# Optimization experiments

Hardware: AMD Instinct MI355X
Metric: run time of the kernel (lower is better)

Reference implementation:

```python
import jax, jax.numpy as jnp
import numpy as np

B, S, D = 4, 2048, 1024
H, A = 16, 64  # num_heads, attention_depth
LN_EPS = 1e-3  # keras LayerNormalization default epsilon


def setup_inputs() -> dict:
    key = jax.random.key(0)
    ks = jax.random.split(key, 12)
    s_in = 1.0 / np.sqrt(D)
    return {
        "query_inputs": jax.random.normal(ks[0], (B, S, D), jnp.float32),
        "key_value_inputs": jax.random.normal(ks[1], (B, S, D), jnp.float32),
        "Wq": jax.random.normal(ks[2], (H, D, A), jnp.float32) * s_in,
        "bq": jnp.zeros((H, A), jnp.float32),
        "Wk": jax.random.normal(ks[3], (H, D, A), jnp.float32) * s_in,
        "bk": jnp.zeros((H, A), jnp.float32),
        "Wo": jax.random.normal(ks[4], (H, D, D), jnp.float32) * s_in,
        "bo": jnp.zeros((H, D), jnp.float32),
        "gamma": jnp.ones((D,), jnp.float32),
        "beta": jnp.zeros((D,), jnp.float32),
    }


def reference(query_inputs, key_value_inputs, Wq, bq, Wk, bk, Wo, bo, gamma, beta):
    sqrt_depth = jnp.sqrt(jnp.asarray(A, jnp.float32))
    # per-head Q/K projections, batched over heads: [B,H,S,A]
    q = (jnp.einsum("bsd,hda->bhsa", query_inputs, Wq) + bq[None, :, None, :]) / sqrt_depth
    k = jnp.einsum("btd,hda->bhta", key_value_inputs, Wk) + bk[None, :, None, :]
    # keras Attention: scores = q @ k^T (q already pre-scaled), causal mask
    scores = jnp.einsum("bhsa,bhta->bhst", q, k)
    causal = jnp.tril(jnp.ones((S, S), bool))
    scores = jnp.where(causal[None, None], scores, jnp.finfo(scores.dtype).min)
    weights = jax.nn.softmax(scores, axis=-1)
    # values are the raw key_value_inputs (model_dims channels)
    attn = jnp.einsum("bhst,btd->bhsd", weights, key_value_inputs)
    # per-head output dense with relu, then sum over heads (tf.add_n)
    head_out = jax.nn.relu(jnp.einsum("bhsd,hde->bhse", attn, Wo) + bo[None, :, None, :])
    attn_sum = head_out.sum(axis=1)  # [B,S,D]
    # dropout is identity in inference mode (training=False)
    x = query_inputs + attn_sum
    mean = x.mean(axis=-1, keepdims=True)
    var = x.var(axis=-1, keepdims=True)
    return gamma * (x - mean) * jax.lax.rsqrt(var + LN_EPS) + beta
```

## Files before the change

### kernel.cpp

```cpp
#include <hip/hip_runtime.h>
#include <stdint.h>

#define B_ 4
#define S_ 2048
#define D_ 1024
#define H_ 16
#define A_ 64
#define LN_EPS 1e-3f
#define L2E 1.4426950408889634f

typedef __bf16 bf16x8 __attribute__((ext_vector_type(8)));
typedef __bf16 bf16x4 __attribute__((ext_vector_type(4)));
typedef float f32x4 __attribute__((ext_vector_type(4)));

__device__ __forceinline__ f32x4 mfma16(bf16x8 a, bf16x8 b, f32x4 c) {
    return __builtin_amdgcn_mfma_f32_16x16x32_bf16(a, b, c, 0, 0, 0);
}
__device__ __forceinline__ void glds16(const void* g, void* l) {
    __builtin_amdgcn_global_load_lds(
        (const __attribute__((address_space(1))) void*)g,
        (__attribute__((address_space(3))) void*)l, 16, 0, 0);
}

#define SWZ(slot, r) ((slot) ^ (((r) & 1) << 2) ^ (((r) >> 1) & 3))
__device__ __forceinline__ void stage_half(const __bf16* __restrict__ src, size_t ld,
                                           __bf16* lhalf, int w, int lane) {
    #pragma unroll
    for (int i = 0; i < 2; ++i) {
        int ch = w * 2 + i;
        int r = ch * 8 + (lane >> 3);
        int sl = SWZ(lane & 7, r);
        glds16(src + (size_t)r * ld + sl * 8, lhalf + ch * 512);
    }
}
__device__ __forceinline__ bf16x8 fragS(const __bf16* h, int r, int ks, int fg) {
    return *(const bf16x8*)(h + r * 64 + SWZ(ks * 4 + fg, r) * 8);
}

__device__ __forceinline__ void glds_tile128(const __bf16* __restrict__ src, size_t ld,
                                             __bf16* lds, int w, int lane) {
    int r = lane >> 2;
    int c = (lane & 3) * 8;
    #pragma unroll
    for (int i = 0; i < 2; ++i) {
        int r0 = (w + i * 4) * 16;
        glds16(src + (size_t)(r0 + r) * ld + c, lds + r0 * 32);
    }
}
template <int NI, int NJ>
__device__ __forceinline__ void mfma_tileL(const __bf16* As, const __bf16* Bs,
                                           int wm, int wn, int fr, int fg,
                                           f32x4 (&acc)[NI][NJ]) {
    bf16x8 af[NI], bv[NJ];
    #pragma unroll
    for (int i = 0; i < NI; ++i)
        af[i] = *(const bf16x8*)(As + (wm + i * 16 + fr) * 32 + fg * 8);
    #pragma unroll
    for (int j = 0; j < NJ; ++j)
        bv[j] = *(const bf16x8*)(Bs + (wn + j * 16 + fr) * 32 + fg * 8);
    #pragma unroll
    for (int i = 0; i < NI; ++i)
        #pragma unroll
        for (int j = 0; j < NJ; ++j)
            acc[i][j] = mfma16(af[i], bv[j], acc[i][j]);
}

__global__ void k_tr_cvt(const float* __restrict__ in, __bf16* __restrict__ out,
                         int R, int C) {
    __shared__ float tile[32][33];
    size_t gbase = (size_t)blockIdx.z * R * C;
    int r0 = blockIdx.y * 32, c0 = blockIdx.x * 32;
    #pragma unroll
    for (int i = threadIdx.y; i < 32; i += 8)
        tile[i][threadIdx.x] = in[gbase + (size_t)(r0 + i) * C + c0 + threadIdx.x];
    __syncthreads();
    #pragma unroll
    for (int i = threadIdx.y; i < 32; i += 8)
        out[gbase + (size_t)(c0 + i) * R + r0 + threadIdx.x] = (__bf16)tile[threadIdx.x][i];
}
__global__ void k_tr_cvt2(const float* __restrict__ in0, const float* __restrict__ in1,
                          __bf16* __restrict__ out0, __bf16* __restrict__ out1,
                          int R, int C) {
    __shared__ float tile[32][33];
    int z = blockIdx.z;
    const float* in = (z < H_) ? in0 : in1;
    __bf16* out = (z < H_) ? out0 : out1;
    size_t gbase = (size_t)(z & (H_ - 1)) * R * C;
    int r0 = blockIdx.y * 32, c0 = blockIdx.x * 32;
    #pragma unroll
    for (int i = threadIdx.y; i < 32; i += 8)
        tile[i][threadIdx.x] = in[gbase + (size_t)(r0 + i) * C + c0 + threadIdx.x];
    __syncthreads();
    #pragma unroll
    for (int i = threadIdx.y; i < 32; i += 8)
        out[gbase + (size_t)(c0 + i) * R + r0 + threadIdx.x] = (__bf16)tile[threadIdx.x][i];
}

__global__ void k_cvt2(const float* __restrict__ in0, const float* __restrict__ in1,
                       __bf16* __restrict__ out0, __bf16* __restrict__ out1, int n8) {
    int i = blockIdx.x * blockDim.x + threadIdx.x;
    if (i >= n8) return;
    const float* in = blockIdx.y ? in1 : in0;
    __bf16* out = blockIdx.y ? out1 : out0;
    const float4* p = (const float4*)(in + (size_t)i * 8);
    float4 f0 = p[0], f1 = p[1];
    __bf16 v[8] = {(__bf16)f0.x, (__bf16)f0.y, (__bf16)f0.z, (__bf16)f0.w,
                   (__bf16)f1.x, (__bf16)f1.y, (__bf16)f1.z, (__bf16)f1.w};
    *(uint4*)(out + (size_t)i * 8) = *(const uint4*)v;
}

__global__ __launch_bounds__(256) void k_proj(
    const __bf16* __restrict__ qb, const __bf16* __restrict__ kvb,
    const __bf16* __restrict__ wqt, const __bf16* __restrict__ wkt,
    const float* __restrict__ bq, const float* __restrict__ bk,
    __bf16* __restrict__ qp, __bf16* __restrict__ kp) {
    __shared__ __bf16 As[2][128 * 32];
    __shared__ __bf16 Bs[2][128 * 32];
    int which = blockIdx.z;
    const __bf16* Ab = which ? kvb : qb;
    const __bf16* Bt = which ? wkt : wqt;
    const float* bias = which ? bk : bq;
    float scale = which ? 1.0f : 0.125f;
    __bf16* outp = which ? kp : qp;
    int m0 = blockIdx.y * 128, n0 = blockIdx.x * 128;
    int t = threadIdx.x, lane = t & 63, w = t >> 6;
    int wm = (w >> 1) * 64, wn = (w & 1) * 64;
    int fr = lane & 15, fg = lane >> 4;
    const __bf16* Abase = Ab + (size_t)m0 * D_;
    const __bf16* Bbase = Bt + (size_t)n0 * D_;
    f32x4 acc[4][4] = {};
    glds_tile128(Abase, D_, As[0], w, lane);
    glds_tile128(Bbase, D_, Bs[0], w, lane);
    __syncthreads();
    int cur = 0;
    const int nt = D_ / 32;
    for (int tt = 0; tt < nt; ++tt) {
        if (tt + 1 < nt) {
            glds_tile128(Abase + (tt + 1) * 32, D_, As[cur ^ 1], w, lane);
            glds_tile128(Bbase + (tt + 1) * 32, D_, Bs[cur ^ 1], w, lane);
        }
        mfma_tileL<4, 4>(As[cur], Bs[cur], wm, wn, fr, fg, acc);
        __syncthreads();
        cur ^= 1;
    }
    #pragma unroll
    for (int j = 0; j < 4; ++j) {
        int n = n0 + wn + j * 16 + fr;
        float bv = bias[n];
        #pragma unroll
        for (int i = 0; i < 4; ++i)
            #pragma unroll
            for (int jj = 0; jj < 4; ++jj) {
                int m = m0 + wm + i * 16 + fg * 4 + jj;
                outp[(size_t)m * (H_ * A_) + n] = (__bf16)((acc[i][j][jj] + bv) * scale);
            }
    }
}

__global__ __launch_bounds__(512, 1) void k_fattn(
    const __bf16* __restrict__ qpb, const __bf16* __restrict__ kpb,
    const __bf16* __restrict__ kvtb, __bf16* __restrict__ att) {
    __shared__ __bf16 Ks[64 * 64];
    __shared__ __bf16 Vs[2][4][128 * 64];
    __shared__ __bf16 Ps[128 * 64];
    __shared__ float lpar[128][2];
    int h = blockIdx.z;
    int yp = blockIdx.y;
    int n0 = blockIdx.x * 512;
    int t = threadIdx.x, lane = t & 63, w = t >> 6;
    int fr = lane & 15, fg = lane >> 4;
    int wr = w >> 2, wc = w & 3;
    int sr = w >> 1, sc = w & 1;
    const __bf16* Vb = kvtb + (size_t)n0 * S_;
    __bf16* ob = att + (size_t)h * S_ * D_;
    int kr = w * 8 + (lane >> 3);
    int ksl = SWZ(lane & 7, kr);

    #pragma unroll 1
    for (int seg = 0; seg < 2; ++seg) {
        int mt = seg ? (15 - yp) : yp;
        int m0 = mt * 128;
        int NT = (mt + 1) * 2;
        stage_half(qpb + (size_t)m0 * (H_ * A_) + h * A_, H_ * A_, Ps, w, lane);
        glds16(kpb + (size_t)kr * (H_ * A_) + h * A_ + ksl * 8, Ks + w * 512);
        asm volatile("s_waitcnt vmcnt(0)" ::: "memory");
        __builtin_amdgcn_s_barrier();
        bf16x8 qf[2][2];
        #pragma unroll
        for (int mi = 0; mi < 2; ++mi)
            #pragma unroll
            for (int ks = 0; ks < 2; ++ks)
                qf[mi][ks] = fragS(Ps, sr * 32 + mi * 16 + fr, ks, fg);
        asm volatile("s_waitcnt lgkmcnt(0)" ::: "memory");
        #pragma unroll
        for (int q = 0; q < 4; ++q)
            stage_half(Vb + (size_t)(q * 128) * S_, S_, &Vs[0][q][0], w, lane);
        uint4 kreg = {0, 0, 0, 0};
        if (NT > 1)
            kreg = *(const uint4*)(kpb + (size_t)(64 + kr) * (H_ * A_) + h * A_ + ksl * 8);
        __builtin_amdgcn_s_barrier();
        __builtin_amdgcn_sched_barrier(0);
        f32x4 acc[4][8] = {};
        float lsum[2][4] = {};
        int cur = 0;
        for (int tt = 0; tt < NT; ++tt) {
            bool pre = (tt + 1 < NT);
            if (pre) {
                asm volatile("s_waitcnt vmcnt(1)" ::: "memory");
            } else {
                asm volatile("s_waitcnt vmcnt(0)" ::: "memory");
            }
            asm volatile("s_waitcnt lgkmcnt(0)" ::: "memory");
            __builtin_amdgcn_s_barrier();
            __builtin_amdgcn_sched_barrier(0);
            f32x4 sac[2][2] = {};
            __builtin_amdgcn_s_setprio(1);
            #pragma unroll
            for (int ks = 0; ks < 2; ++ks)
                #pragma unroll
                for (int nj = 0; nj < 2; ++nj) {
                    bf16x8 kf = fragS(Ks, sc * 32 + nj * 16 + fr, ks, fg);
                    #pragma unroll
                    for (int mi = 0; mi < 2; ++mi)
                        sac[mi][nj] = mfma16(qf[mi][ks], kf, sac[mi][nj]);
                }
            __builtin_amdgcn_s_setprio(0);
            bool dg = (tt >= 2 * mt);
            #pragma unroll
            for (int mi = 0; mi < 2; ++mi)
                #pragma unroll
                for (int nj = 0; nj < 2; ++nj)
                    #pragma unroll
                    for (int jj = 0; jj < 4; ++jj) {
                        int srow = sr * 32 + mi * 16 + fg * 4 + jj;
                        int col = sc * 32 + nj * 16 + fr;
                        float p = exp2f(sac[mi][nj][jj] * L2E);
                        if (dg && (tt * 64 + col > m0 + srow)) p = 0.f;
                        lsum[mi][jj] += p;
                        Ps[srow * 64 + (col ^ (fg << 4))] = (__bf16)p;
                    }
            asm volatile("s_waitcnt lgkmcnt(0)" ::: "memory");
            __builtin_amdgcn_s_barrier();
            __builtin_amdgcn_sched_barrier(0);
            if (pre) {
                #pragma unroll
                for (int q = 0; q < 4; ++q)
                    stage_half(Vb + (size_t)(q * 128) * S_ + (tt + 1) * 64, S_,
                               &Vs[cur ^ 1][q][0], w, lane);
                asm volatile("s_waitcnt vmcnt(8)" ::: "memory");
                *(uint4*)(Ks + w * 512 + lane * 8) = kreg;
                if (tt + 2 < NT)
                    kreg = *(const uint4*)(kpb + (size_t)((tt + 2) * 64 + kr) * (H_ * A_) +
                                           h * A_ + ksl * 8);
            }
            __builtin_amdgcn_s_setprio(1);
            const __bf16* Vh = &Vs[cur][wc][0];
            #pragma unroll
            for (int ks = 0; ks < 2; ++ks) {
                bf16x8 pa[4], vf[8];
                #pragma unroll
                for (int mi = 0; mi < 4; ++mi) {
                    int r = wr * 64 + mi * 16 + fr;
                    int g = (ks * 4 + fg) ^ (((fr >> 2) & 3) << 1);
                    pa[mi] = *(const bf16x8*)(Ps + r * 64 + g * 8);
                }
                #pragma unroll
                for (int nj = 0; nj < 8; ++nj)
                    vf[nj] = fragS(Vh, nj * 16 + fr, ks, fg);
                #pragma unroll
                for (int mi = 0; mi < 4; ++mi)
                    #pragma unroll
                    for (int nj = 0; nj < 8; ++nj)
                        acc[mi][nj] = mfma16(pa[mi], vf[nj], acc[mi][nj]);
            }
            __builtin_amdgcn_s_setprio(0);
            __builtin_amdgcn_sched_barrier(0);
            cur ^= 1;
        }
        #pragma unroll
        for (int mi = 0; mi < 2; ++mi)
            #pragma unroll
            for (int jj = 0; jj < 4; ++jj) {
                float v = lsum[mi][jj];
                v += __shfl_xor(v, 1);
                v += __shfl_xor(v, 2);
                v += __shfl_xor(v, 4);
                v += __shfl_xor(v, 8);
                if (fr == 0) lpar[sr * 32 + mi * 16 + fg * 4 + jj][sc] = v;
            }
        asm volatile("s_waitcnt lgkmcnt(0)" ::: "memory");
        __builtin_amdgcn_s_barrier();
        #pragma unroll
        for (int mi = 0; mi < 4; ++mi)
            #pragma unroll
            for (int jj = 0; jj < 4; ++jj) {
                int row = wr * 64 + mi * 16 + fg * 4 + jj;
                float il = 1.f / (lpar[row][0] + lpar[row][1]);
                int m = m0 + row;
                #pragma unroll
                for (int nj = 0; nj < 8; ++nj) {
                    int n = n0 + wc * 128 + nj * 16 + fr;
                    ob[(size_t)m * D_ + n] = (__bf16)(acc[mi][nj][jj] * il);
                }
            }
        __builtin_amdgcn_s_barrier();
    }
}

__global__ __launch_bounds__(512) void k_headsum(
    const __bf16* __restrict__ att, const __bf16* __restrict__ Wot,
    const float* __restrict__ bo, __bf16* __restrict__ asum) {
    __shared__ __bf16 L[2][4][8192];
    int p = blockIdx.z;
    int mt = blockIdx.y, n0 = blockIdx.x * 256;
    int m0 = mt * 256;
    int t = threadIdx.x, lane = t & 63, w = t >> 6;
    int wr = w >> 2, wc = w & 3;
    int fr = lane & 15, fg = lane >> 4;
    const __bf16* Ab = att + ((size_t)p * S_ + m0) * D_;
    const __bf16* Bb = Wot + ((size_t)p * D_ + n0) * D_;
    float bv4[4];
    #pragma unroll
    for (int j = 0; j < 4; ++j)
        bv4[j] = bo[(size_t)p * D_ + n0 + wc * 64 + j * 16 + fr];
    f32x4 acc[8][4] = {};
    auto stg = [&](int tt, int h, int buf) {
        const __bf16* s = (h < 2) ? (Ab + (size_t)(h * 128) * D_ + tt * 64)
                                  : (Bb + (size_t)((h - 2) * 128) * D_ + tt * 64);
        stage_half(s, D_, &L[buf][h][0], w, lane);
    };
    auto loads = [&](const __bf16* Ah, const __bf16* Bh, int rb0, int mh, int nh,
                     bf16x8 (&af)[4][2], bf16x8 (&bv)[2][2]) {
        #pragma unroll
        for (int i = 0; i < 4; ++i)
            #pragma unroll
            for (int ks = 0; ks < 2; ++ks)
                af[i][ks] = fragS(Ah, mh * 64 + i * 16 + fr, ks, fg);
        #pragma unroll
        for (int j = 0; j < 2; ++j)
            #pragma unroll
            for (int ks = 0; ks < 2; ++ks)
                bv[j][ks] = fragS(Bh, rb0 + nh * 32 + j * 16 + fr, ks, fg);
    };
    stg(0, 0, 0); stg(0, 1, 0); stg(0, 2, 0); stg(0, 3, 0);
    int cur = 0;
    const int nt = D_ / 64;
    for (int tt = 0; tt < nt; ++tt) {
        bool pre = (tt + 1 < nt);
        const __bf16* Ah = &L[cur][wr][0];
        const __bf16* Bh = &L[cur][2 + (wc >> 1)][0];
        int rb0 = (wc & 1) * 64;
        #pragma unroll
        for (int ph = 0; ph < 4; ++ph) {
            const int mh = ph >> 1, nh = ph & 1;
            bf16x8 af[4][2], bv[2][2];
            if (ph == 0) {
                if (pre) {
                    stg(tt + 1, 0, cur ^ 1);
                    stg(tt + 1, 1, cur ^ 1);
                    stg(tt + 1, 2, cur ^ 1);
                    stg(tt + 1, 3, cur ^ 1);
                    asm volatile("s_waitcnt vmcnt(8)" ::: "memory");
                } else {
                    asm volatile("s_waitcnt vmcnt(0)" ::: "memory");
                }
                __builtin_amdgcn_s_barrier();
                __builtin_amdgcn_sched_barrier(0);
                loads(Ah, Bh, rb0, mh, nh, af, bv);
            } else {
                loads(Ah, Bh, rb0, mh, nh, af, bv);
                __builtin_amdgcn_s_barrier();
                __builtin_amdgcn_sched_barrier(0);
            }
            __builtin_amdgcn_s_setprio(1);
            #pragma unroll
            for (int i = 0; i < 4; ++i)
                #pragma unroll
                for (int j = 0; j < 2; ++j) {
                    acc[mh * 4 + i][nh * 2 + j] =
                        mfma16(af[i][0], bv[j][0], acc[mh * 4 + i][nh * 2 + j]);
                    acc[mh * 4 + i][nh * 2 + j] =
                        mfma16(af[i][1], bv[j][1], acc[mh * 4 + i][nh * 2 + j]);
                }
            __builtin_amdgcn_s_setprio(0);
            __builtin_amdgcn_sched_barrier(0);
            __builtin_amdgcn_s_barrier();
        }
        cur ^= 1;
    }
    __bf16* dst = asum + ((size_t)p * S_ + m0) * D_;
    #pragma unroll
    for (int mi = 0; mi < 8; ++mi)
        #pragma unroll
        for (int jj = 0; jj < 4; ++jj) {
            int mr = wr * 128 + mi * 16 + fg * 4 + jj;
            #pragma unroll
            for (int nj = 0; nj < 4; ++nj) {
                int nc = n0 + wc * 64 + nj * 16 + fr;
                dst[(size_t)mr * D_ + nc] = (__bf16)fmaxf(acc[mi][nj][jj] + bv4[nj], 0.f);
            }
        }
}

__global__ __launch_bounds__(256) void k_ln(
    const float* __restrict__ x1b, const __bf16* __restrict__ parts,
    const float* __restrict__ gamma, const float* __restrict__ beta,
    float* __restrict__ outb) {
    int row = blockIdx.x;
    size_t base = (size_t)row * D_;
    int c = threadIdx.x * 4;
    float4 a = *(const float4*)(x1b + base + c);
    float x[4] = {a.x, a.y, a.z, a.w};
    #pragma unroll
    for (int p = 0; p < H_; ++p) {
        bf16x4 v = *(const bf16x4*)(parts + ((size_t)p * S_ + row) * D_ + c);
        x[0] += (float)v[0]; x[1] += (float)v[1];
        x[2] += (float)v[2]; x[3] += (float)v[3];
    }
    float sm = x[0] + x[1] + x[2] + x[3];
    float s2 = x[0] * x[0] + x[1] * x[1] + x[2] * x[2] + x[3] * x[3];
    #pragma unroll
    for (int m = 32; m >= 1; m >>= 1) {
        sm += __shfl_xor(sm, m);
        s2 += __shfl_xor(s2, m);
    }
    __shared__ float r1[4], r2[4];
    int w = threadIdx.x >> 6;
    if ((threadIdx.x & 63) == 0) { r1[w] = sm; r2[w] = s2; }
    __syncthreads();
    sm = r1[0] + r1[1] + r1[2] + r1[3];
    s2 = r2[0] + r2[1] + r2[2] + r2[3];
    float mean = sm * (1.f / D_);
    float var = s2 * (1.f / D_) - mean * mean;
    float rstd = rsqrtf(var + LN_EPS);
    #pragma unroll
    for (int jj = 0; jj < 4; ++jj)
        outb[base + c + jj] = gamma[c + jj] * (x[jj] - mean) * rstd + beta[c + jj];
}

extern "C" void kernel_launch(void* const* d_in, const int* in_sizes, int n_in,
                              void* d_out, int out_size, void* d_ws, size_t ws_size,
                              hipStream_t stream) {
    (void)in_sizes; (void)n_in; (void)out_size; (void)ws_size;
    const float* qin   = (const float*)d_in[0];
    const float* kvin  = (const float*)d_in[1];
    const float* Wq    = (const float*)d_in[2];
    const float* bq    = (const float*)d_in[3];
    const float* Wk    = (const float*)d_in[4];
    const float* bk    = (const float*)d_in[5];
    const float* Wo    = (const float*)d_in[6];
    const float* bo    = (const float*)d_in[7];
    const float* gamma = (const float*)d_in[8];
    const float* beta  = (const float*)d_in[9];
    float* out = (float*)d_out;
    char* ws = (char*)d_ws;

    size_t off = 0;
    auto alloc = [&](size_t bytes) {
        size_t o = off;
        off += (bytes + 255) & ~(size_t)255;
        return o;
    };
    size_t o_wqt = alloc((size_t)H_ * A_ * D_ * 2);
    size_t o_wkt = alloc((size_t)H_ * A_ * D_ * 2);
    size_t o_wot = alloc((size_t)H_ * D_ * D_ * 2);
    size_t o_kvt = alloc((size_t)B_ * D_ * S_ * 2);
    size_t o_qp  = alloc((size_t)B_ * S_ * H_ * A_ * 2);
    size_t o_kp  = alloc((size_t)B_ * S_ * H_ * A_ * 2);
    size_t o_att = alloc((size_t)H_ * S_ * D_ * 2);
    size_t xbytes_qb = (size_t)B_ * S_ * D_ * 2 * 2;
    size_t xbytes_as = (size_t)H_ * S_ * D_ * 2;
    size_t o_x = alloc(xbytes_qb > xbytes_as ? xbytes_qb : xbytes_as);

    __bf16* wqt = (__bf16*)(ws + o_wqt);
    __bf16* wkt = (__bf16*)(ws + o_wkt);
    __bf16* wot = (__bf16*)(ws + o_wot);
    __bf16* kvt = (__bf16*)(ws + o_kvt);
    __bf16* qp  = (__bf16*)(ws + o_qp);
    __bf16* kp  = (__bf16*)(ws + o_kp);
    __bf16* att = (__bf16*)(ws + o_att);
    __bf16* qb  = (__bf16*)(ws + o_x);
    __bf16* kvb = qb + (size_t)B_ * S_ * D_;
    __bf16* asum = (__bf16*)(ws + o_x);

    k_tr_cvt2<<<dim3(A_ / 32, D_ / 32, 2 * H_), dim3(32, 8), 0, stream>>>(
        Wq, Wk, wqt, wkt, D_, A_);
    k_tr_cvt<<<dim3(D_ / 32, D_ / 32, H_), dim3(32, 8), 0, stream>>>(Wo, wot, D_, D_);
    k_tr_cvt<<<dim3(D_ / 32, S_ / 32, B_), dim3(32, 8), 0, stream>>>(kvin, kvt, S_, D_);
    int n8 = B_ * S_ * D_ / 8;
    k_cvt2<<<dim3((n8 + 255) / 256, 2), 256, 0, stream>>>(qin, kvin, qb, kvb, n8);
    k_proj<<<dim3(8, 64, 2), 256, 0, stream>>>(qb, kvb, wqt, wkt, bq, bk, qp, kp);

    for (int b = 0; b < B_; ++b) {
        const __bf16* qpb  = qp + (size_t)b * S_ * (H_ * A_);
        const __bf16* kpb  = kp + (size_t)b * S_ * (H_ * A_);
        const __bf16* kvtb = kvt + (size_t)b * D_ * S_;
        k_fattn<<<dim3(D_ / 512, 8, H_), 512, 0, stream>>>(qpb, kpb, kvtb, att);
        k_headsum<<<dim3(D_ / 256, S_ / 256, H_), 512, 0, stream>>>(att, wot, bo, asum);
        k_ln<<<S_, 256, 0, stream>>>(qin + (size_t)b * S_ * D_, asum, gamma, beta,
                                     out + (size_t)b * S_ * D_);
    }
}
```

Baseline: 1.143 ms.

## Remap attention and headsum blocks per XCD, issue V prefetch earlier, split mask path

Both the flash-attention and head-sum kernels now use a 1D grid and remap block IDs so blocks sharing a head (and its K/V or Wo tiles) land on the same XCD. This is meant to improve L2 locality across the chiplets. The V-tile prefetch for the next iteration is issued before the QK^T MFMAs instead of after the softmax barrier, so the global loads get more time to overlap with compute. The softmax loop is also split into masked (diagonal) and unmasked variants, which drops the per-element mask check on off-diagonal tiles but adds code size.

Result: faster. 1.044 ms (-8.6%).

```diff
diff --git a/kernel.cpp b/kernel.cpp
--- a/kernel.cpp
+++ b/kernel.cpp
@@ -164,9 +164,11 @@
     __shared__ __bf16 Vs[2][4][128 * 64];
     __shared__ __bf16 Ps[128 * 64];
     __shared__ float lpar[128][2];
-    int h = blockIdx.z;
-    int yp = blockIdx.y;
-    int n0 = blockIdx.x * 512;
+    int bid = blockIdx.x;
+    int xcd = bid & 7, slot = bid >> 3;
+    int n0 = (xcd & 1) * 512;
+    int h = (xcd >> 1) * 4 + (slot >> 3);
+    int yp = slot & 7;
     int t = threadIdx.x, lane = t & 63, w = t >> 6;
     int fr = lane & 15, fg = lane >> 4;
     int wr = w >> 2, wc = w & 3;
@@ -213,6 +215,12 @@
             asm volatile("s_waitcnt lgkmcnt(0)" ::: "memory");
             __builtin_amdgcn_s_barrier();
             __builtin_amdgcn_sched_barrier(0);
+            if (pre) {
+                #pragma unroll
+                for (int q = 0; q < 4; ++q)
+                    stage_half(Vb + (size_t)(q * 128) * S_ + (tt + 1) * 64, S_,
+                               &Vs[cur ^ 1][q][0], w, lane);
+            }
             f32x4 sac[2][2] = {};
             __builtin_amdgcn_s_setprio(1);
             #pragma unroll
@@ -226,27 +234,38 @@
                 }
             __builtin_amdgcn_s_setprio(0);
             bool dg = (tt >= 2 * mt);
-            #pragma unroll
-            for (int mi = 0; mi < 2; ++mi)
-                #pragma unroll
-                for (int nj = 0; nj < 2; ++nj)
+            if (dg) {
+                #pragma unroll
+                for (int mi = 0; mi < 2; ++mi)
                     #pragma unroll
-                    for (int jj = 0; jj < 4; ++jj) {
-                        int srow = sr * 32 + mi * 16 + fg * 4 + jj;
-                        int col = sc * 32 + nj * 16 + fr;
-                        float p = exp2f(sac[mi][nj][jj] * L2E);
-                        if (dg && (tt * 64 + col > m0 + srow)) p = 0.f;
-                        lsum[mi][jj] += p;
-                        Ps[srow * 64 + (col ^ (fg << 4))] = (__bf16)p;
-                    }
+                    for (int nj = 0; nj < 2; ++nj)
+                        #pragma unroll
+                        for (int jj = 0; jj < 4; ++jj) {
+                            int srow = sr * 32 + mi * 16 + fg * 4 + jj;
+                            int col = sc * 32 + nj * 16 + fr;
+                            float p = exp2f(sac[mi][nj][jj] * L2E);
+                            if (tt * 64 + col > m0 + srow) p = 0.f;
+                            lsum[mi][jj] += p;
+                            Ps[srow * 64 + (col ^ (fg << 4))] = (__bf16)p;
+                        }
+            } else {
+                #pragma unroll
+                for (int mi = 0; mi < 2; ++mi)
+                    #pragma unroll
+                    for (int nj = 0; nj < 2; ++nj)
+                        #pragma unroll
+                        for (int jj = 0; jj < 4; ++jj) {
+                            int srow = sr * 32 + mi * 16 + fg * 4 + jj;
+                            int col = sc * 32 + nj * 16 + fr;
+                            float p = exp2f(sac[mi][nj][jj] * L2E);
+                            lsum[mi][jj] += p;
+                            Ps[srow * 64 + (col ^ (fg << 4))] = (__bf16)p;
+                        }
+            }
             asm volatile("s_waitcnt lgkmcnt(0)" ::: "memory");
             __builtin_amdgcn_s_barrier();
             __builtin_amdgcn_sched_barrier(0);
             if (pre) {
-                #pragma unroll
-                for (int q = 0; q < 4; ++q)
-                    stage_half(Vb + (size_t)(q * 128) * S_ + (tt + 1) * 64, S_,
-                               &Vs[cur ^ 1][q][0], w, lane);
                 asm volatile("s_waitcnt vmcnt(8)" ::: "memory");
                 *(uint4*)(Ks + w * 512 + lane * 8) = kreg;
                 if (tt + 2 < NT)
@@ -311,8 +330,12 @@
     const __bf16* __restrict__ att, const __bf16* __restrict__ Wot,
     const float* __restrict__ bo, __bf16* __restrict__ asum) {
     __shared__ __bf16 L[2][4][8192];
-    int p = blockIdx.z;
-    int mt = blockIdx.y, n0 = blockIdx.x * 256;
+    int bid = blockIdx.x;
+    int xcd = bid & 7, slot = bid >> 3;
+    int p = xcd * 2 + (slot >> 5);
+    int rem = slot & 31;
+    int mt = rem >> 2;
+    int n0 = (rem & 3) * 256;
     int m0 = mt * 256;
     int t = threadIdx.x, lane = t & 63, w = t >> 6;
     int wr = w >> 2, wc = w & 3;
@@ -495,8 +518,8 @@
         const __bf16* qpb  = qp + (size_t)b * S_ * (H_ * A_);
         const __bf16* kpb  = kp + (size_t)b * S_ * (H_ * A_);
         const __bf16* kvtb = kvt + (size_t)b * D_ * S_;
-        k_fattn<<<dim3(D_ / 512, 8, H_), 512, 0, stream>>>(qpb, kpb, kvtb, att);
-        k_headsum<<<dim3(D_ / 256, S_ / 256, H_), 512, 0, stream>>>(att, wot, bo, asum);
+        k_fattn<<<256, 512, 0, stream>>>(qpb, kpb, kvtb, att);
+        k_headsum<<<512, 512, 0, stream>>>(att, wot, bo, asum);
         k_ln<<<S_, 256, 0, stream>>>(qin + (size_t)b * S_ * D_, asum, gamma, beta,
                                      out + (size_t)b * S_ * D_);
     }
```
